# Optimization experiments

Measured on AMD Instinct MI355X. Metric: run time of the kernel, lower is better.

The kernel has to match this reference:

```python
import jax, jax.numpy as jnp
import numpy as np

OUT_C, IN_C, K = 64, 64, 3
H, W = 32, 32


def setup_inputs() -> dict:
    key = jax.random.key(0)
    k1, k2, k3 = jax.random.split(key, 3)
    x = jax.random.normal(k1, (1, H, W, IN_C), dtype=jnp.float32)
    # One rational activation (P5/Q4, PAU 'version A') per (out_c, in_c, ky, kx)
    w_num = jax.random.normal(k2, (OUT_C, IN_C, K, K, 6), dtype=jnp.float32) * 0.1
    w_den = jax.random.normal(k3, (OUT_C, IN_C, K, K, 4), dtype=jnp.float32) * 0.1
    return {"x": x, "w_num": w_num, "w_den": w_den}


def reference(x, w_num, w_den):
    # x: [1, H, W, C] -- original module only supports batch=1 (squeeze semantics)
    h, w, c = x.shape[1], x.shape[2], x.shape[3]
    pad = (K - 1) // 2
    xp = jnp.pad(x[0], ((pad, pad), (pad, pad), (0, 0)))  # [H+2p, W+2p, C]
    # patches[a,b,i,j,c] = xp[i+a, j+b, c]  (same 'same-padding' sliding window)
    patches = jnp.stack(
        [jnp.stack([xp[a:a + h, b:b + w, :] for b in range(K)], axis=0)
         for a in range(K)], axis=0)  # [K,K,H,W,C]
    # powers x^0..x^5, computed once and reused by numerator and denominator
    pows = jnp.stack([patches ** n for n in range(6)], axis=0)  # [6,K,K,H,W,C]
    # per (f,c,a,b) rational: P(x) = sum_n a_n x^n,  Q(x) = 1 + |sum_{n=1..4} b_n x^n|
    P = jnp.einsum('nabijc,fcabn->fabijc', pows, w_num)
    Q = 1.0 + jnp.abs(jnp.einsum('nabijc,fcabn->fabijc', pows[1:5], w_den))
    # sum contributions over kernel positions (a,b) and input channels c
    return jnp.sum(P / Q, axis=(1, 2, 5))  # [OUT_C, H, W]
```

## Files before the change

### kernel.cpp

```cpp
#include <hip/hip_runtime.h>
#include <math.h>

#define NOUT 64
#define NIN  64
#define HH   32
#define WW   32
#define PADH 34
#define PADW 34
#define PIXW 8

#define XP_ELEMS  (PADH * PADW * NIN)
#define NREC      (NOUT * 9 * NIN)
#define WPK_ELEMS (NREC * 12)

__global__ __launch_bounds__(256) void prep_kernel(const float* __restrict__ x,
                                                   const float* __restrict__ wn,
                                                   const float* __restrict__ wd,
                                                   float* __restrict__ xp,
                                                   float* __restrict__ wpk) {
    int idx = blockIdx.x * 256 + threadIdx.x;
    if (idx < XP_ELEMS) {
        int c  = idx & 63;
        int t  = idx >> 6;
        int jj = t % PADW;
        int ii = t / PADW;
        float v = 0.0f;
        if (ii >= 1 && ii <= HH && jj >= 1 && jj <= WW)
            v = x[((ii - 1) * WW + (jj - 1)) * NIN + c];
        xp[idx] = v;
    } else {
        int t  = idx - XP_ELEMS;
        int c  = t & 63;
        int ab = (t >> 6) % 9;
        int f  = t / (9 * 64);
        const float* sn = wn + ((f * NIN + c) * 9 + ab) * 6;
        const float* sd = wd + ((f * NIN + c) * 9 + ab) * 4;
        float* dst = wpk + ((size_t)((f * 9 + ab) * 64 + c)) * 12;
        dst[0] = sn[0]; dst[1] = sn[1]; dst[2]  = sn[2]; dst[3]  = sn[3];
        dst[4] = sn[4]; dst[5] = sn[5]; dst[6]  = sd[0]; dst[7]  = sd[1];
        dst[8] = sd[2]; dst[9] = sd[3]; dst[10] = 0.0f;  dst[11] = 0.0f;
    }
}

__global__ __launch_bounds__(256) void kan_main(const float* __restrict__ xp,
                                                const float* __restrict__ wpk,
                                                float* __restrict__ out) {
    int bid  = blockIdx.x;
    int wgid = (bid & 7) * 256 + (bid >> 3);
    int wv   = wgid * 4 + (threadIdx.x >> 6);
    int lane = threadIdx.x & 63;
    int f    = wv >> 7;
    int rem  = wv & 127;
    int i    = rem >> 2;
    int j0   = (rem & 3) * PIXW;

    float acc[PIXW];
#pragma unroll
    for (int p = 0; p < PIXW; ++p) acc[p] = 0.0f;

    const float4* wr = (const float4*)(wpk + ((size_t)(f * 9) * 64 + lane) * 12);

#pragma unroll 3
    for (int ab = 0; ab < 9; ++ab) {
        const int a = ab / 3, b = ab % 3;
        float4 wA = wr[ab * 192 + 0];
        float4 wB = wr[ab * 192 + 1];
        float4 wC = wr[ab * 192 + 2];

        const float* xb = xp + ((i + a) * PADW + (j0 + b)) * NIN + lane;
#pragma unroll
        for (int p = 0; p < PIXW; ++p) {
            float xv = xb[p * NIN];
            float pn = fmaf(wB.y, xv, wB.x);
            pn = fmaf(pn, xv, wA.w);
            pn = fmaf(pn, xv, wA.z);
            pn = fmaf(pn, xv, wA.y);
            pn = fmaf(pn, xv, wA.x);
            float qn = fmaf(wC.y, xv, wC.x);
            qn = fmaf(qn, xv, wB.w);
            qn = fmaf(qn, xv, wB.z);
            float den = 1.0f + fabsf(xv * qn);
            acc[p] = fmaf(pn, __builtin_amdgcn_rcpf(den), acc[p]);
        }
    }

#pragma unroll
    for (int p = 0; p < PIXW; ++p) {
        float s = acc[p];
        s += __shfl_xor(s, 32, 64);
        s += __shfl_xor(s, 16, 64);
        s += __shfl_xor(s, 8, 64);
        s += __shfl_xor(s, 4, 64);
        s += __shfl_xor(s, 2, 64);
        s += __shfl_xor(s, 1, 64);
        if (lane == p) out[f * (HH * WW) + i * WW + j0 + p] = s;
    }
}

__global__ __launch_bounds__(256) void kan_fallback(const float* __restrict__ x,
                                                    const float* __restrict__ wn,
                                                    const float* __restrict__ wd,
                                                    float* __restrict__ out) {
    __shared__ float red[256];
    int bid = blockIdx.x;
    int t = bid & 15;
    int f = bid >> 4;
    int tid = threadIdx.x;
    int g = tid >> 6;
    int p = tid & 63;
    int r = p >> 5;
    int j = p & 31;
    int i = t * 2 + r;
    int c0 = g * 16;
    const float* wnb = wn + (f * NIN + c0) * 9 * 6;
    const float* wdb = wd + (f * NIN + c0) * 9 * 4;
    float acc = 0.0f;
    for (int c = 0; c < 16; ++c) {
        float xv[9];
#pragma unroll
        for (int a = 0; a < 3; ++a)
#pragma unroll
            for (int b = 0; b < 3; ++b) {
                int ii = i + a - 1, jj = j + b - 1;
                bool inb = (ii >= 0) && (ii < HH) && (jj >= 0) && (jj < WW);
                xv[a * 3 + b] = inb ? x[(ii * WW + jj) * NIN + (c0 + c)] : 0.0f;
            }
        const float* wnc = wnb + c * 54;
        const float* wdc = wdb + c * 36;
#pragma unroll
        for (int ab = 0; ab < 9; ++ab) {
            float xx = xv[ab];
            float pn = fmaf(wnc[ab * 6 + 5], xx, wnc[ab * 6 + 4]);
            pn = fmaf(pn, xx, wnc[ab * 6 + 3]);
            pn = fmaf(pn, xx, wnc[ab * 6 + 2]);
            pn = fmaf(pn, xx, wnc[ab * 6 + 1]);
            pn = fmaf(pn, xx, wnc[ab * 6 + 0]);
            float qn = fmaf(wdc[ab * 4 + 3], xx, wdc[ab * 4 + 2]);
            qn = fmaf(qn, xx, wdc[ab * 4 + 1]);
            qn = fmaf(qn, xx, wdc[ab * 4 + 0]);
            float den = 1.0f + fabsf(xx * qn);
            acc = fmaf(pn, __builtin_amdgcn_rcpf(den), acc);
        }
    }
    red[tid] = acc;
    __syncthreads();
    if (tid < 64) {
        float s = red[tid] + red[tid + 64] + red[tid + 128] + red[tid + 192];
        int rr = tid >> 5;
        int jj = tid & 31;
        out[f * (HH * WW) + (t * 2 + rr) * WW + jj] = s;
    }
}

extern "C" void kernel_launch(void* const* d_in, const int* in_sizes, int n_in,
                              void* d_out, int out_size, void* d_ws, size_t ws_size,
                              hipStream_t stream) {
    const float* x  = (const float*)d_in[0];
    const float* wn = (const float*)d_in[1];
    const float* wd = (const float*)d_in[2];
    float* out = (float*)d_out;

    const size_t need = (size_t)(XP_ELEMS + WPK_ELEMS) * sizeof(float);

    if (ws_size >= need) {
        float* xp  = (float*)d_ws;
        float* wpk = xp + XP_ELEMS;
        const int prep_total = XP_ELEMS + NREC;
        prep_kernel<<<prep_total / 256, 256, 0, stream>>>(x, wn, wd, xp, wpk);
        kan_main<<<2048, 256, 0, stream>>>(xp, wpk, out);
    } else {
        kan_fallback<<<NOUT * 16, 256, 0, stream>>>(x, wn, wd, out);
    }
}
```

Baseline: 27.55 us.

## Stage padded input band in LDS and repack weights with coalesced reads

The separate padded-input buffer is dropped. Each 512-thread block now loads a 4-row padded band of x into shared memory, handling halo zeros inline, and computes two output rows for one output channel from LDS. The weight packing kernel is rewritten so each thread copies one source word, which makes reads coalesced, and the pad slots are no longer zeroed. The cost is a larger block with a barrier and redundant halo loads across blocks, and the grid and block shape change (1024 blocks of 512 threads).

Measured after the change: 28.08 us. Within noise of the previous version (+1.9%).

```diff
diff --git a/kernel.cpp b/kernel.cpp
--- a/kernel.cpp
+++ b/kernel.cpp
@@ -5,72 +5,88 @@
 #define NIN  64
 #define HH   32
 #define WW   32
-#define PADH 34
-#define PADW 34
-#define PIXW 8
 
-#define XP_ELEMS  (PADH * PADW * NIN)
 #define NREC      (NOUT * 9 * NIN)
 #define WPK_ELEMS (NREC * 12)
+#define WN_WORDS  (NOUT * NIN * 9 * 6)
+#define WD_WORDS  (NOUT * NIN * 9 * 4)
 
-__global__ __launch_bounds__(256) void prep_kernel(const float* __restrict__ x,
-                                                   const float* __restrict__ wn,
-                                                   const float* __restrict__ wd,
-                                                   float* __restrict__ xp,
-                                                   float* __restrict__ wpk) {
+__global__ __launch_bounds__(256) void wpack_kernel(const float* __restrict__ wn,
+                                                    const float* __restrict__ wd,
+                                                    float* __restrict__ wpk) {
     int idx = blockIdx.x * 256 + threadIdx.x;
-    if (idx < XP_ELEMS) {
-        int c  = idx & 63;
-        int t  = idx >> 6;
-        int jj = t % PADW;
-        int ii = t / PADW;
-        float v = 0.0f;
-        if (ii >= 1 && ii <= HH && jj >= 1 && jj <= WW)
-            v = x[((ii - 1) * WW + (jj - 1)) * NIN + c];
-        xp[idx] = v;
+    if (idx < WN_WORDS) {
+        int n  = idx % 6;
+        int t  = idx / 6;
+        int ab = t % 9;
+        int t2 = t / 9;
+        int c  = t2 & 63;
+        int f  = t2 >> 6;
+        wpk[((f * 9 + ab) * 64 + c) * 12 + n] = wn[idx];
     } else {
-        int t  = idx - XP_ELEMS;
-        int c  = t & 63;
-        int ab = (t >> 6) % 9;
-        int f  = t / (9 * 64);
-        const float* sn = wn + ((f * NIN + c) * 9 + ab) * 6;
-        const float* sd = wd + ((f * NIN + c) * 9 + ab) * 4;
-        float* dst = wpk + ((size_t)((f * 9 + ab) * 64 + c)) * 12;
-        dst[0] = sn[0]; dst[1] = sn[1]; dst[2]  = sn[2]; dst[3]  = sn[3];
-        dst[4] = sn[4]; dst[5] = sn[5]; dst[6]  = sd[0]; dst[7]  = sd[1];
-        dst[8] = sd[2]; dst[9] = sd[3]; dst[10] = 0.0f;  dst[11] = 0.0f;
+        int id2 = idx - WN_WORDS;
+        int n  = id2 & 3;
+        int t  = id2 >> 2;
+        int ab = t % 9;
+        int t2 = t / 9;
+        int c  = t2 & 63;
+        int f  = t2 >> 6;
+        wpk[((f * 9 + ab) * 64 + c) * 12 + 6 + n] = wd[id2];
     }
 }
 
-__global__ __launch_bounds__(256) void kan_main(const float* __restrict__ xp,
-                                                const float* __restrict__ wpk,
-                                                float* __restrict__ out) {
+__global__ __launch_bounds__(512, 8) void kan_main(const float* __restrict__ x,
+                                                   const float* __restrict__ wpk,
+                                                   float* __restrict__ out) {
+    __shared__ float xt[4 * 34 * 64];
+
     int bid  = blockIdx.x;
-    int wgid = (bid & 7) * 256 + (bid >> 3);
-    int wv   = wgid * 4 + (threadIdx.x >> 6);
-    int lane = threadIdx.x & 63;
-    int f    = wv >> 7;
-    int rem  = wv & 127;
-    int i    = rem >> 2;
-    int j0   = (rem & 3) * PIXW;
+    int wgid = (bid & 7) * 128 + (bid >> 3);
+    int f    = wgid >> 4;
+    int band = wgid & 15;
+    int i0   = band * 2;
 
-    float acc[PIXW];
+    int tid  = threadIdx.x;
+    int lane = tid & 63;
+    int wave = tid >> 6;
+
 #pragma unroll
-    for (int p = 0; p < PIXW; ++p) acc[p] = 0.0f;
+    for (int k = 0; k < 17; ++k) {
+        int idx = k * 512 + tid;
+        int c   = idx & 63;
+        int pos = idx >> 6;
+        int col = pos % 34;
+        int t   = pos / 34;
+        int gi  = i0 - 1 + t;
+        int gj  = col - 1;
+        float v = 0.0f;
+        if (gi >= 0 && gi < HH && gj >= 0 && gj < WW)
+            v = x[(gi * WW + gj) * NIN + c];
+        xt[idx] = v;
+    }
+    __syncthreads();
 
-    const float4* wr = (const float4*)(wpk + ((size_t)(f * 9) * 64 + lane) * 12);
+    int wr = wave >> 2;
+    int j0 = (wave & 3) * 8;
+    int i  = i0 + wr;
 
-#pragma unroll 3
+    float acc[8];
+#pragma unroll
+    for (int p = 0; p < 8; ++p) acc[p] = 0.0f;
+
+    const float4* w4 = (const float4*)(wpk + ((size_t)(f * 9) * 64 + lane) * 12);
+
+#pragma unroll 2
     for (int ab = 0; ab < 9; ++ab) {
         const int a = ab / 3, b = ab % 3;
-        float4 wA = wr[ab * 192 + 0];
-        float4 wB = wr[ab * 192 + 1];
-        float4 wC = wr[ab * 192 + 2];
+        float4 wA = w4[ab * 192 + 0];
+        float4 wB = w4[ab * 192 + 1];
+        float4 wC = w4[ab * 192 + 2];
 
-        const float* xb = xp + ((i + a) * PADW + (j0 + b)) * NIN + lane;
+        const float* xb = &xt[((wr + a) * 34 + (j0 + b)) * 64 + lane];
 #pragma unroll
-        for (int p = 0; p < PIXW; ++p) {
-            float xv = xb[p * NIN];
+        for (int p = 0; p < 8; ++p) {
+            float xv = xb[p * 64];
             float pn = fmaf(wB.y, xv, wB.x);
             pn = fmaf(pn, xv, wA.w);
             pn = fmaf(pn, xv, wA.z);
@@ -85,7 +101,7 @@
     }
 
 #pragma unroll
-    for (int p = 0; p < PIXW; ++p) {
+    for (int p = 0; p < 8; ++p) {
         float s = acc[p];
         s += __shfl_xor(s, 32, 64);
         s += __shfl_xor(s, 16, 64);
@@ -160,14 +176,13 @@
     const float* wd = (const float*)d_in[2];
     float* out = (float*)d_out;
 
-    const size_t need = (size_t)(XP_ELEMS + WPK_ELEMS) * sizeof(float);
+    const size_t need = (size_t)WPK_ELEMS * sizeof(float);
 
     if (ws_size >= need) {
-        float* xp  = (float*)d_ws;
-        float* wpk = xp + XP_ELEMS;
-        const int prep_total = XP_ELEMS + NREC;
-        prep_kernel<<<prep_total / 256, 256, 0, stream>>>(x, wn, wd, xp, wpk);
-        kan_main<<<2048, 256, 0, stream>>>(xp, wpk, out);
+        float* wpk = (float*)d_ws;
+        const int pack_total = WN_WORDS + WD_WORDS;
+        wpack_kernel<<<pack_total / 256, 256, 0, stream>>>(wn, wd, wpk);
+        kan_main<<<1024, 512, 0, stream>>>(x, wpk, out);
     } else {
         kan_fallback<<<NOUT * 16, 256, 0, stream>>>(x, wn, wd, out);
     }
```
